# Kernel optimization log

Measured on AMD Instinct MI355X. Metric: run time of the kernel, lower is better.

The kernel has to match this reference:

```python
import jax, jax.numpy as jnp
import numpy as np

D_MODEL = 1024
N_HEADS = 16
D_FF = 4096
B = 8
S_TGT = 1024
S_SRC = 1024


def layer_norm(x, g, b, eps=1e-5):
    mu = jnp.mean(x, axis=-1, keepdims=True)
    var = jnp.mean(jnp.square(x - mu), axis=-1, keepdims=True)
    return (x - mu) * jax.lax.rsqrt(var + eps) * g + b


def mha(q_in, k_in, v_in, Wq, bq, Wk, bk, Wv, bv, Wo, bo, mask):
    Bq, Sq, D = q_in.shape
    hd = D // N_HEADS

    def split(t):
        return t.reshape(t.shape[0], t.shape[1], N_HEADS, hd).transpose(0, 2, 1, 3)

    Q = split(q_in @ Wq + bq)   # [B,H,Sq,hd]
    K = split(k_in @ Wk + bk)   # [B,H,Sk,hd]
    V = split(v_in @ Wv + bv)
    scores = jnp.einsum('bhqd,bhkd->bhqk', Q, K) / jnp.sqrt(jnp.float32(hd))
    scores = jnp.where(mask, scores, jnp.float32(-1e9))
    attn = jax.nn.softmax(scores, axis=-1)
    out = jnp.einsum('bhqk,bhkd->bhqd', attn, V)
    out = out.transpose(0, 2, 1, 3).reshape(Bq, Sq, D)
    return out @ Wo + bo


def setup_inputs() -> dict:
    key = jax.random.key(0)
    ks = jax.random.split(key, 32)
    s = 0.02
    inp = {
        'x': jax.random.normal(ks[0], (B, S_TGT, D_MODEL), dtype=jnp.float32),
        'encoder_output': jax.random.normal(ks[1], (B, S_SRC, D_MODEL), dtype=jnp.float32),
        'tgt_mask': jnp.tril(jnp.ones((S_TGT, S_TGT), dtype=bool))[None, None],
        'src_mask': jnp.ones((1, 1, S_TGT, S_SRC), dtype=bool),
    }
    i = 2
    for p in ('sa', 'ca'):
        for w in ('Wq', 'Wk', 'Wv', 'Wo'):
            inp[f'{p}_{w}'] = jax.random.normal(ks[i], (D_MODEL, D_MODEL), dtype=jnp.float32) * s
            inp[f'{p}_b{w[1].lower()}'] = jnp.zeros((D_MODEL,), dtype=jnp.float32)
            i += 1
    inp['ff_W1'] = jax.random.normal(ks[i], (D_MODEL, D_FF), dtype=jnp.float32) * s; i += 1
    inp['ff_b1'] = jnp.zeros((D_FF,), dtype=jnp.float32)
    inp['ff_W2'] = jax.random.normal(ks[i], (D_FF, D_MODEL), dtype=jnp.float32) * s; i += 1
    inp['ff_b2'] = jnp.zeros((D_MODEL,), dtype=jnp.float32)
    for n in ('ln1', 'ln2', 'ln3'):
        inp[f'{n}_g'] = jnp.ones((D_MODEL,), dtype=jnp.float32)
        inp[f'{n}_b'] = jnp.zeros((D_MODEL,), dtype=jnp.float32)
    return inp


def reference(x, encoder_output, tgt_mask, src_mask,
              sa_Wq, sa_bq, sa_Wk, sa_bk, sa_Wv, sa_bv, sa_Wo, sa_bo,
              ca_Wq, ca_bq, ca_Wk, ca_bk, ca_Wv, ca_bv, ca_Wo, ca_bo,
              ff_W1, ff_b1, ff_W2, ff_b2,
              ln1_g, ln1_b, ln2_g, ln2_b, ln3_g, ln3_b):
    # masked self-attention + residual + LN (dropout = identity in eval mode)
    attn = mha(x, x, x, sa_Wq, sa_bq, sa_Wk, sa_bk, sa_Wv, sa_bv, sa_Wo, sa_bo, tgt_mask)
    x = layer_norm(x + attn, ln1_g, ln1_b)
    # cross-attention to encoder output
    cross = mha(x, encoder_output, encoder_output,
                ca_Wq, ca_bq, ca_Wk, ca_bk, ca_Wv, ca_bv, ca_Wo, ca_bo, src_mask)
    x = layer_norm(x + cross, ln2_g, ln2_b)
    # position-wise FFN: Linear -> ReLU -> Linear
    ff = jax.nn.relu(x @ ff_W1 + ff_b1) @ ff_W2 + ff_b2
    x = layer_norm(x + ff, ln3_g, ln3_b)
    return x
```

## Files before the change

kernel.cpp:

```cpp
#include <hip/hip_runtime.h>
#include <math.h>

typedef __attribute__((ext_vector_type(8))) short short8;
typedef __attribute__((ext_vector_type(4))) short short4v;
typedef __attribute__((ext_vector_type(4))) float floatx4;

__device__ inline float bf2f(unsigned short h) {
    unsigned int u = ((unsigned int)h) << 16;
    float f;
    __builtin_memcpy(&f, &u, 4);
    return f;
}
__device__ inline unsigned short f2bf(float f) {
    unsigned int u;
    __builtin_memcpy(&u, &f, 4);
    u = (u + 0x7fffu + ((u >> 16) & 1u)) >> 16;
    return (unsigned short)u;
}
__device__ inline unsigned int f2u(float f) {
    return __builtin_bit_cast(unsigned int, f);
}

__device__ inline void gld_lds16(const unsigned short* g, unsigned short* l) {
    __builtin_amdgcn_global_load_lds(
        (const __attribute__((address_space(1))) unsigned int*)g,
        (__attribute__((address_space(3))) unsigned int*)l, 16, 0, 0);
}

__global__ __launch_bounds__(256) void detect_dtype(
    const unsigned short* __restrict__ x, int* __restrict__ flag) {
    __shared__ int s[4];
    int bad = 0;
    for (int i = threadIdx.x; i < 8192; i += 256) {
        float v = bf2f(x[i]);
        if (!(fabsf(v) <= 1.0e4f)) bad = 1;
    }
    unsigned long long b = __ballot(bad);
    int wave = threadIdx.x >> 6;
    if ((threadIdx.x & 63) == 0) s[wave] = (b != 0ULL) ? 1 : 0;
    __syncthreads();
    if (threadIdx.x == 0) flag[0] = s[0] | s[1] | s[2] | s[3];
}

__global__ __launch_bounds__(256) void to_bf16_kernel(
    const void* __restrict__ in, unsigned short* __restrict__ out,
    const int* __restrict__ flag, int n8) {
    int fl = flag[0];
    int i = blockIdx.x * 256 + threadIdx.x;
    if (i >= n8) return;
    size_t off = (size_t)i * 8;
    if (fl) {
        floatx4 f0 = *(const floatx4*)((const float*)in + off);
        floatx4 f1 = *(const floatx4*)((const float*)in + off + 4);
        short8 v;
#pragma unroll
        for (int j = 0; j < 4; j++) {
            v[j] = (short)f2bf(f0[j]);
            v[4 + j] = (short)f2bf(f1[j]);
        }
        *(short8*)(out + off) = v;
    } else {
        *(short8*)(out + off) = *(const short8*)((const unsigned short*)in + off);
    }
}

__global__ __launch_bounds__(256) void transpose_any(
    const void* __restrict__ in, unsigned short* __restrict__ out,
    int rows, int cols, const int* __restrict__ flag) {
    int fl = flag ? flag[0] : 0;
    __shared__ unsigned short t[32][33];
    int tx = threadIdx.x & 31, ty = threadIdx.x >> 5;
    int c0 = blockIdx.x * 32, r0 = blockIdx.y * 32;
    size_t base = (size_t)blockIdx.z * rows * cols;
#pragma unroll
    for (int k = 0; k < 4; k++) {
        size_t idx = base + (size_t)(r0 + ty + k * 8) * cols + c0 + tx;
        t[ty + k * 8][tx] = fl ? f2bf(((const float*)in)[idx])
                               : ((const unsigned short*)in)[idx];
    }
    __syncthreads();
#pragma unroll
    for (int k = 0; k < 4; k++)
        out[base + (size_t)(c0 + ty + k * 8) * rows + r0 + tx] = t[tx][ty + k * 8];
}

struct Ptr8 { const void* p[8]; };
__global__ __launch_bounds__(256) void transpose8(
    Ptr8 in, unsigned short* __restrict__ out, const int* __restrict__ flag) {
    int fl = flag[0];
    __shared__ unsigned short t[32][33];
    const void* src = in.p[blockIdx.z];
    unsigned short* dst = out + (size_t)blockIdx.z * 1024 * 1024;
    int tx = threadIdx.x & 31, ty = threadIdx.x >> 5;
    int c0 = blockIdx.x * 32, r0 = blockIdx.y * 32;
#pragma unroll
    for (int k = 0; k < 4; k++) {
        size_t idx = (size_t)(r0 + ty + k * 8) * 1024 + c0 + tx;
        t[ty + k * 8][tx] = fl ? f2bf(((const float*)src)[idx])
                               : ((const unsigned short*)src)[idx];
    }
    __syncthreads();
#pragma unroll
    for (int k = 0; k < 4; k++)
        dst[(size_t)(c0 + ty + k * 8) * 1024 + r0 + tx] = t[tx][ty + k * 8];
}

__device__ inline void stage_half(const unsigned short* __restrict__ G, int ldk,
                                  int grow, int gcol, unsigned short* ldsb,
                                  int tid) {
    int s0 = tid, s1 = tid + 512;
    int r0 = s0 >> 3, c0 = ((s0 & 7) ^ (r0 & 7)) << 3;
    int r1 = s1 >> 3, c1 = ((s1 & 7) ^ (r1 & 7)) << 3;
    gld_lds16(&G[(size_t)(grow + r0) * ldk + gcol + c0], &ldsb[s0 * 8]);
    gld_lds16(&G[(size_t)(grow + r1) * ldk + gcol + c1], &ldsb[s1 * 8]);
}

template <int BN_, int EPI>
__global__ __launch_bounds__(512) void gemm8(
    const unsigned short* __restrict__ A, const unsigned short* __restrict__ Bt,
    const void* __restrict__ b0, const void* __restrict__ b1,
    const void* __restrict__ b2, unsigned short* __restrict__ C0,
    unsigned short* __restrict__ C1, unsigned short* __restrict__ C2,
    int M, int N, int K, const int* __restrict__ flag) {
    constexpr int NR = BN_ / 64;
    constexpr int WNT = BN_ / 4;
    constexpr int ASZ = 16384;
    constexpr int BSZ = BN_ * 64;
    __shared__ alignas(16) unsigned short lds[2 * ASZ + 2 * BSZ];

    const int tid = threadIdx.x;
    const int lane = tid & 63, wave = tid >> 6;
    const int quad = lane >> 4, l16 = lane & 15, x7 = l16 & 7;
    const int wm = wave >> 2, wn = wave & 3;
    const int bm = blockIdx.x * 256, bn = blockIdx.y * BN_;
    const int NT = K >> 6;

    floatx4 acc[8][NR];
#pragma unroll
    for (int i = 0; i < 8; ++i)
#pragma unroll
        for (int j = 0; j < NR; ++j) acc[i][j] = (floatx4){0.f, 0.f, 0.f, 0.f};

    stage_half(A, K, bm, 0, lds, tid);
    stage_half(A, K, bm + 128, 0, lds + 8192, tid);
    stage_half(Bt, K, bn, 0, lds + 2 * ASZ, tid);
    if (BN_ == 256) stage_half(Bt, K, bn + 128, 0, lds + 2 * ASZ + 8192, tid);
    asm volatile("s_waitcnt vmcnt(0)" ::: "memory");
    __builtin_amdgcn_s_barrier();

    short8 bfr[NR][2], afr[2][2][2];

    for (int it = 0; it < NT; ++it) {
        unsigned short* const Ac = lds + (it & 1) * ASZ;
        unsigned short* const Bc = lds + 2 * ASZ + (it & 1) * BSZ;
        unsigned short* const An = lds + ((it + 1) & 1) * ASZ;
        unsigned short* const Bn = lds + 2 * ASZ + ((it + 1) & 1) * BSZ;
        const bool more = (it + 1 < NT);
        if (more) {
            const int kn = (it + 1) << 6;
            stage_half(A, K, bm, kn, An, tid);
            stage_half(A, K, bm + 128, kn, An + 8192, tid);
            stage_half(Bt, K, bn, kn, Bn, tid);
            if (BN_ == 256) stage_half(Bt, K, bn + 128, kn, Bn + 8192, tid);
        }
#pragma unroll
        for (int ni = 0; ni < NR; ++ni)
#pragma unroll
            for (int ks = 0; ks < 2; ++ks)
                bfr[ni][ks] = *(const short8*)&Bc[
                    (wn * WNT + ni * 16 + l16) * 64 +
                    ((((ks << 2) + quad) ^ x7) << 3)];
#pragma unroll
        for (int m2 = 0; m2 < 2; ++m2)
#pragma unroll
            for (int ks = 0; ks < 2; ++ks)
                afr[0][m2][ks] = *(const short8*)&Ac[
                    (wm * 128 + m2 * 16 + l16) * 64 +
                    ((((ks << 2) + quad) ^ x7) << 3)];
#pragma unroll
        for (int q = 0; q < 4; ++q) {
            if (q < 3) {
#pragma unroll
                for (int m2 = 0; m2 < 2; ++m2)
#pragma unroll
                    for (int ks = 0; ks < 2; ++ks)
                        afr[(q + 1) & 1][m2][ks] = *(const short8*)&Ac[
                            (wm * 128 + ((q + 1) * 2 + m2) * 16 + l16) * 64 +
                            ((((ks << 2) + quad) ^ x7) << 3)];
            }
            __builtin_amdgcn_s_setprio(1);
#pragma unroll
            for (int m2 = 0; m2 < 2; ++m2)
#pragma unroll
                for (int ni = 0; ni < NR; ++ni) {
                    acc[q * 2 + m2][ni] = __builtin_amdgcn_mfma_f32_16x16x32_bf16(
                        bfr[ni][0], afr[q & 1][m2][0], acc[q * 2 + m2][ni], 0, 0, 0);
                    acc[q * 2 + m2][ni] = __builtin_amdgcn_mfma_f32_16x16x32_bf16(
                        bfr[ni][1], afr[q & 1][m2][1], acc[q * 2 + m2][ni], 0, 0, 0);
                }
            __builtin_amdgcn_s_setprio(0);
        }
        if (more) {
            asm volatile("s_waitcnt vmcnt(0)" ::: "memory");
            __builtin_amdgcn_s_barrier();
        }
    }

    const int fl = flag[0];
    const void* bp = b0;
    unsigned short* Cp = C0;
    int mode = 0;
    int cb = bn;
    if (EPI == 1) mode = 1;
    if (EPI == 4) mode = 2;
    if (EPI == 2) {
        int ch = bn >> 10;
        cb = bn & 1023;
        bp = (ch == 0) ? b0 : (ch == 1) ? b1 : b2;
        Cp = (ch == 0) ? C0 : (ch == 1) ? C1 : C2;
        mode = (ch == 0) ? 2 : (ch == 1) ? 3 : 4;
    }
    if (EPI == 3) {
        int ch = bn >> 10;
        cb = bn & 1023;
        bp = (ch == 0) ? b0 : b1;
        Cp = (ch == 0) ? C0 : C1;
        mode = (ch == 0) ? 3 : 4;
    }
#pragma unroll
    for (int ni = 0; ni < NR; ++ni) {
        const int colb = cb + wn * WNT + ni * 16 + quad * 4;
        float b4[4];
        if (fl) {
            floatx4 t = *(const floatx4*)&((const float*)bp)[colb];
#pragma unroll
            for (int r = 0; r < 4; ++r) b4[r] = t[r];
        } else {
            short4v t = *(const short4v*)&((const unsigned short*)bp)[colb];
#pragma unroll
            for (int r = 0; r < 4; ++r) b4[r] = bf2f((unsigned short)t[r]);
        }
        const int hh = colb >> 6, dd = colb & 63;
#pragma unroll
        for (int mi = 0; mi < 8; ++mi) {
            const int row = bm + wm * 128 + mi * 16 + l16;
            short4v pk;
#pragma unroll
            for (int r = 0; r < 4; ++r) {
                float v = acc[mi][ni][r] + b4[r];
                if (mode == 1) v = fmaxf(v, 0.f);
                if (mode == 2) v *= 0.18033688f;
                pk[r] = (short)f2bf(v);
            }
            if (mode <= 1) {
                *(short4v*)&Cp[(size_t)row * N + colb] = pk;
            } else {
                const int b_ = row >> 10, s_ = row & 1023;
                if (mode != 4) {
                    *(short4v*)&Cp[((((size_t)b_ * 16 + hh) * 1024) + s_) * 64 + dd] = pk;
                } else {
#pragma unroll
                    for (int r = 0; r < 4; ++r)
                        Cp[(((size_t)b_ * 16 + hh) * 64 + dd + r) * 1024 + s_] =
                            (unsigned short)pk[r];
                }
            }
        }
    }
}

template <int CAUSAL>
__global__ __launch_bounds__(256) void attn_kernel(
    const unsigned short* __restrict__ Q, const unsigned short* __restrict__ K,
    const unsigned short* __restrict__ Vt, unsigned short* __restrict__ O,
    int Skv) {
    __shared__ alignas(16) unsigned short Ks[2][512 * 8];
    __shared__ alignas(16) unsigned short Vs[2][512 * 8];
    const int S = 1024;
    int tid = threadIdx.x, wave = tid >> 6, lane = tid & 63;
    int quad = lane >> 4, l16 = lane & 15;
    int fid = blockIdx.y * 8 + blockIdx.x;
    int bh = fid & 127;
    int qt = fid >> 7;
    if (CAUSAL) qt = 7 - qt;
    int qbA = qt * 128 + wave * 32;
    int qbB = qbA + 16;
    const unsigned short* Qp = Q + (size_t)bh * S * 64;
    const unsigned short* Kp = K + (size_t)bh * Skv * 64;
    const unsigned short* Vp = Vt + (size_t)bh * 64 * Skv;

    short8 qA0 = *(const short8*)&Qp[(qbA + l16) * 64 + quad * 8];
    short8 qA1 = *(const short8*)&Qp[(qbA + l16) * 64 + 32 + quad * 8];
    short8 qB0 = *(const short8*)&Qp[(qbB + l16) * 64 + quad * 8];
    short8 qB1 = *(const short8*)&Qp[(qbB + l16) * 64 + 32 + quad * 8];

    floatx4 oA[4], oB[4];
#pragma unroll
    for (int ni = 0; ni < 4; ni++) {
        oA[ni] = (floatx4){0.f, 0.f, 0.f, 0.f};
        oB[ni] = (floatx4){0.f, 0.f, 0.f, 0.f};
    }
    float mA = -1e30f, lA = 0.f, mB = -1e30f, lB = 0.f;
    const int kend = CAUSAL ? (qt + 1) * 128 : Skv;
    const int nch = kend >> 6;

    int sr0 = tid >> 3, sc0 = (tid & 7) ^ (sr0 & 7);
    int sr1 = (tid + 256) >> 3, sc1 = ((tid + 256) & 7) ^ (sr1 & 7);
    int shA = l16 + (((2 * quad) & 3) << 4);
    int shB = l16 + (((2 * quad + 1) & 3) << 4);

    short8 vone;
    {
        unsigned int dw[4] = {0x3F803F80u, 0x3F803F80u, 0x3F803F80u, 0x3F803F80u};
        __builtin_memcpy(&vone, dw, 16);
    }

    auto stageKV = [&](int kb, int b) {
        gld_lds16(&Kp[(size_t)(kb + sr0) * 64 + sc0 * 8], &Ks[b][tid * 8]);
        gld_lds16(&Kp[(size_t)(kb + sr1) * 64 + sc1 * 8], &Ks[b][(tid + 256) * 8]);
        gld_lds16(&Vp[(size_t)sr0 * Skv + kb + sc0 * 8], &Vs[b][tid * 8]);
        gld_lds16(&Vp[(size_t)sr1 * Skv + kb + sc1 * 8], &Vs[b][(tid + 256) * 8]);
    };

    stageKV(0, 0);
    asm volatile("s_waitcnt vmcnt(0)" ::: "memory");
    __builtin_amdgcn_s_barrier();

    for (int ic = 0; ic < nch; ++ic) {
        const int kb = ic << 6, cur = ic & 1;
        const unsigned short* Ksc = Ks[cur];
        const unsigned short* Vsc = Vs[cur];
        if (ic + 1 < nch) stageKV(kb + 64, cur ^ 1);

        const bool doA = !CAUSAL || (kb <= qbA + 15);
        const bool doB = !CAUSAL || (kb <= qbB + 15);

        if (doB) {
            floatx4 stA[4], stB[4];
            __builtin_amdgcn_s_setprio(1);
#pragma unroll
            for (int c = 0; c < 4; c++) {
                int row = c * 16 + l16, r7 = row & 7;
                short8 kf0 = *(const short8*)&Ksc[(row * 8 + (quad ^ r7)) * 8];
                short8 kf1 = *(const short8*)&Ksc[(row * 8 + ((quad + 4) ^ r7)) * 8];
                if (doA) {
                    floatx4 z = (floatx4){0.f, 0.f, 0.f, 0.f};
                    z = __builtin_amdgcn_mfma_f32_16x16x32_bf16(kf0, qA0, z, 0, 0, 0);
                    z = __builtin_amdgcn_mfma_f32_16x16x32_bf16(kf1, qA1, z, 0, 0, 0);
                    stA[c] = z;
                }
                floatx4 y = (floatx4){0.f, 0.f, 0.f, 0.f};
                y = __builtin_amdgcn_mfma_f32_16x16x32_bf16(kf0, qB0, y, 0, 0, 0);
                y = __builtin_amdgcn_mfma_f32_16x16x32_bf16(kf1, qB1, y, 0, 0, 0);
                stB[c] = y;
            }
            __builtin_amdgcn_s_setprio(0);

            auto softmax_pack = [&](floatx4(&st)[4], float& m, float& l,
                                    floatx4(&o)[4], short8(&pf)[2], int qb) {
                if (CAUSAL && (kb + 63 > qb)) {
#pragma unroll
                    for (int c = 0; c < 4; c++)
#pragma unroll
                        for (int r = 0; r < 4; r++) {
                            int kk = kb + c * 16 + quad * 4 + r;
                            if (kk > qb + l16) st[c][r] = -1e30f;
                        }
                }
                float t0 = fmaxf(fmaxf(st[0][0], st[0][1]), st[0][2]);
                float t1 = fmaxf(fmaxf(st[0][3], st[1][0]), st[1][1]);
                float t2 = fmaxf(fmaxf(st[1][2], st[1][3]), st[2][0]);
                float t3 = fmaxf(fmaxf(st[2][1], st[2][2]), st[2][3]);
                float t4 = fmaxf(fmaxf(st[3][0], st[3][1]), st[3][2]);
                float smax = fmaxf(fmaxf(fmaxf(t0, t1), fmaxf(t2, t3)),
                                   fmaxf(t4, st[3][3]));
                smax = fmaxf(smax, __shfl_xor(smax, 16));
                smax = fmaxf(smax, __shfl_xor(smax, 32));
                float mi = m;
                if (!__all(smax <= m + 8.f)) {
                    mi = fmaxf(m, smax);
                    float alpha = exp2f(m - mi);
                    l *= alpha;
#pragma unroll
                    for (int ni = 0; ni < 4; ni++) o[ni] *= alpha;
                    m = mi;
                }
#pragma unroll
                for (int c = 0; c < 4; c++)
#pragma unroll
                    for (int r = 0; r < 4; r++) st[c][r] = exp2f(st[c][r] - mi);
                unsigned int pd[4][2];
#pragma unroll
                for (int c = 0; c < 4; c++) {
                    pd[c][0] = __builtin_amdgcn_perm(f2u(st[c][1]), f2u(st[c][0]),
                                                     0x07060302u);
                    pd[c][1] = __builtin_amdgcn_perm(f2u(st[c][3]), f2u(st[c][2]),
                                                     0x07060302u);
                }
#pragma unroll
                for (int h = 0; h < 2; h++) {
                    unsigned int a0 = __shfl((int)pd[2 * h][0], shA);
                    unsigned int a1 = __shfl((int)pd[2 * h][1], shA);
                    unsigned int a2 = __shfl((int)pd[2 * h][0], shB);
                    unsigned int a3 = __shfl((int)pd[2 * h][1], shB);
                    unsigned int b0 = __shfl((int)pd[2 * h + 1][0], shA);
                    unsigned int b1 = __shfl((int)pd[2 * h + 1][1], shA);
                    unsigned int b2 = __shfl((int)pd[2 * h + 1][0], shB);
                    unsigned int b3 = __shfl((int)pd[2 * h + 1][1], shB);
                    unsigned int dw[4];
                    dw[0] = (quad < 2) ? a0 : b0;
                    dw[1] = (quad < 2) ? a1 : b1;
                    dw[2] = (quad < 2) ? a2 : b2;
                    dw[3] = (quad < 2) ? a3 : b3;
                    __builtin_memcpy(&pf[h], dw, 16);
                }
            };

            short8 pfA[2], pfB[2];
            if (doA) softmax_pack(stA, mA, lA, oA, pfA, qbA);
            softmax_pack(stB, mB, lB, oB, pfB, qbB);

            __builtin_amdgcn_s_setprio(1);
            if (doA) {
                floatx4 zA = (floatx4){0.f, 0.f, 0.f, 0.f};
                zA = __builtin_amdgcn_mfma_f32_16x16x32_bf16(vone, pfA[0], zA, 0, 0, 0);
                zA = __builtin_amdgcn_mfma_f32_16x16x32_bf16(vone, pfA[1], zA, 0, 0, 0);
                lA += zA[0];
            }
            {
                floatx4 zB = (floatx4){0.f, 0.f, 0.f, 0.f};
                zB = __builtin_amdgcn_mfma_f32_16x16x32_bf16(vone, pfB[0], zB, 0, 0, 0);
                zB = __builtin_amdgcn_mfma_f32_16x16x32_bf16(vone, pfB[1], zB, 0, 0, 0);
                lB += zB[0];
            }
#pragma unroll
            for (int ni = 0; ni < 4; ni++) {
                int row = ni * 16 + l16, r7 = row & 7;
                short8 vf0 = *(const short8*)&Vsc[(row * 8 + (quad ^ r7)) * 8];
                short8 vf1 = *(const short8*)&Vsc[(row * 8 + ((quad + 4) ^ r7)) * 8];
                if (doA) {
                    oA[ni] = __builtin_amdgcn_mfma_f32_16x16x32_bf16(vf0, pfA[0], oA[ni], 0, 0, 0);
                    oA[ni] = __builtin_amdgcn_mfma_f32_16x16x32_bf16(vf1, pfA[1], oA[ni], 0, 0, 0);
                }
                oB[ni] = __builtin_amdgcn_mfma_f32_16x16x32_bf16(vf0, pfB[0], oB[ni], 0, 0, 0);
                oB[ni] = __builtin_amdgcn_mfma_f32_16x16x32_bf16(vf1, pfB[1], oB[ni], 0, 0, 0);
            }
            __builtin_amdgcn_s_setprio(0);
        }

        if (ic + 1 < nch) {
            asm volatile("s_waitcnt vmcnt(0)" ::: "memory");
            __builtin_amdgcn_s_barrier();
        }
    }

    int b = bh >> 4, h = bh & 15;
    float invA = 1.0f / lA, invB = 1.0f / lB;
    size_t qrowA = ((size_t)(b * S + qbA + l16)) * 1024 + h * 64;
    size_t qrowB = ((size_t)(b * S + qbB + l16)) * 1024 + h * 64;
#pragma unroll
    for (int ni = 0; ni < 4; ni++) {
        short4v p4;
#pragma unroll
        for (int r = 0; r < 4; r++) p4[r] = (short)f2bf(oA[ni][r] * invA);
        *(short4v*)&O[qrowA + ni * 16 + quad * 4] = p4;
#pragma unroll
        for (int r = 0; r < 4; r++) p4[r] = (short)f2bf(oB[ni][r] * invB);
        *(short4v*)&O[qrowB + ni * 16 + quad * 4] = p4;
    }
}

template <int AEXT, int OEXT>
__global__ __launch_bounds__(256) void add_ln_kernel(
    const void* __restrict__ A, const unsigned short* __restrict__ Bv,
    const void* __restrict__ g, const void* __restrict__ be,
    void* __restrict__ out, const int* __restrict__ flag) {
    int fl = flag[0];
    __shared__ float red[2][4];
    int row = blockIdx.x, tid = threadIdx.x;
    size_t base = (size_t)row * 1024;
    int c = tid * 4;
    float v[4], sum = 0.f, ss = 0.f;
    if (AEXT && fl) {
        floatx4 af = *(const floatx4*)&((const float*)A)[base + c];
#pragma unroll
        for (int k = 0; k < 4; k++) v[k] = af[k];
    } else {
        short4v av = *(const short4v*)&((const unsigned short*)A)[base + c];
#pragma unroll
        for (int k = 0; k < 4; k++) v[k] = bf2f((unsigned short)av[k]);
    }
    short4v bv = *(const short4v*)&Bv[base + c];
#pragma unroll
    for (int k = 0; k < 4; k++) {
        v[k] += bf2f((unsigned short)bv[k]);
        sum += v[k];
        ss += v[k] * v[k];
    }
#pragma unroll
    for (int off = 1; off < 64; off <<= 1) {
        sum += __shfl_xor(sum, off);
        ss += __shfl_xor(ss, off);
    }
    int wave = tid >> 6, lane = tid & 63;
    if (lane == 0) {
        red[0][wave] = sum;
        red[1][wave] = ss;
    }
    __syncthreads();
    sum = red[0][0] + red[0][1] + red[0][2] + red[0][3];
    ss = red[1][0] + red[1][1] + red[1][2] + red[1][3];
    float mu = sum * (1.0f / 1024.0f);
    float var = ss * (1.0f / 1024.0f) - mu * mu;
    float rstd = rsqrtf(var + 1e-5f);
#pragma unroll
    for (int k = 0; k < 4; k++) {
        float gv = fl ? ((const float*)g)[c + k]
                      : bf2f(((const unsigned short*)g)[c + k]);
        float bev = fl ? ((const float*)be)[c + k]
                       : bf2f(((const unsigned short*)be)[c + k]);
        float y = (v[k] - mu) * rstd * gv + bev;
        if (OEXT && fl)
            ((float*)out)[base + c + k] = y;
        else
            ((unsigned short*)out)[base + c + k] = f2bf(y);
    }
}

extern "C" void kernel_launch(void* const* d_in, const int* in_sizes, int n_in,
                              void* d_out, int out_size, void* d_ws, size_t ws_size,
                              hipStream_t stream) {
    const int M = 8192;
    typedef const void* cvp;
    cvp x = d_in[0];
    cvp enc = d_in[1];
    cvp saWq = d_in[4], sabq = d_in[5];
    cvp saWk = d_in[6], sabk = d_in[7];
    cvp saWv = d_in[8], sabv = d_in[9];
    cvp saWo = d_in[10], sabo = d_in[11];
    cvp caWq = d_in[12], cabq = d_in[13];
    cvp caWk = d_in[14], cabk = d_in[15];
    cvp caWv = d_in[16], cabv = d_in[17];
    cvp caWo = d_in[18], cabo = d_in[19];
    cvp ffW1 = d_in[20], ffb1 = d_in[21];
    cvp ffW2 = d_in[22], ffb2 = d_in[23];
    cvp ln1g = d_in[24], ln1b = d_in[25];
    cvp ln2g = d_in[26], ln2b = d_in[27];
    cvp ln3g = d_in[28], ln3b = d_in[29];

    char* ws = (char*)d_ws;
    const size_t MB = 1024 * 1024;
    typedef unsigned short* up;
    up wt_sa_qkv = (up)(ws + 0);
    up wt_sa_o   = (up)(ws + 6 * MB);
    up wt_ca_q   = (up)(ws + 8 * MB);
    up wt_ca_kv  = (up)(ws + 10 * MB);
    up wt_ca_o   = (up)(ws + 14 * MB);
    up wtff1     = (up)(ws + 16 * MB);
    up wtff2     = (up)(ws + 24 * MB);
    up Qb  = (up)(ws + 32 * MB);
    up Kb  = (up)(ws + 48 * MB);
    up Vtb = (up)(ws + 64 * MB);
    up xb  = (up)(ws + 80 * MB);
    up Hb  = (up)(ws + 32 * MB);
    up Ob  = (up)(ws + 96 * MB);
    up Pb  = (up)(ws + 112 * MB);
    up x1  = (up)(ws + 128 * MB);
    up x2  = (up)(ws + 144 * MB);
    up encb = (up)(ws + 144 * MB);
    int* flag = (int*)(ws + 160 * MB);

    dim3 blk(256), blk5(512);
    detect_dtype<<<1, blk, 0, stream>>>((const unsigned short*)x, flag);

    to_bf16_kernel<<<4096, blk, 0, stream>>>(x, xb, flag, M * 1024 / 8);
    to_bf16_kernel<<<4096, blk, 0, stream>>>(enc, encb, flag, M * 1024 / 8);

    Ptr8 w8;
    w8.p[0] = saWq; w8.p[1] = saWk; w8.p[2] = saWv; w8.p[3] = saWo;
    w8.p[4] = caWq; w8.p[5] = caWk; w8.p[6] = caWv; w8.p[7] = caWo;
    transpose8<<<dim3(32, 32, 8), blk, 0, stream>>>(w8, (up)(ws + 0), flag);
    transpose_any<<<dim3(128, 32, 1), blk, 0, stream>>>(ffW1, wtff1, 1024, 4096, flag);
    transpose_any<<<dim3(32, 128, 1), blk, 0, stream>>>(ffW2, wtff2, 4096, 1024, flag);

    gemm8<256, 2><<<dim3(32, 12), blk5, 0, stream>>>(
        xb, wt_sa_qkv, sabq, sabk, sabv, Qb, Kb, Vtb, M, 3072, 1024, flag);
    attn_kernel<1><<<dim3(8, 128), blk, 0, stream>>>(Qb, Kb, Vtb, Ob, 1024);
    gemm8<128, 0><<<dim3(32, 8), blk5, 0, stream>>>(
        Ob, wt_sa_o, sabo, nullptr, nullptr, Pb, nullptr, nullptr, M, 1024, 1024, flag);
    add_ln_kernel<1, 0><<<dim3(8192), blk, 0, stream>>>(x, Pb, ln1g, ln1b, x1, flag);

    gemm8<128, 4><<<dim3(32, 8), blk5, 0, stream>>>(
        x1, wt_ca_q, cabq, nullptr, nullptr, Qb, nullptr, nullptr, M, 1024, 1024, flag);
    gemm8<256, 3><<<dim3(32, 8), blk5, 0, stream>>>(
        encb, wt_ca_kv, cabk, cabv, nullptr, Kb, Vtb, nullptr, M, 2048, 1024, flag);
    attn_kernel<0><<<dim3(8, 128), blk, 0, stream>>>(Qb, Kb, Vtb, Ob, 1024);
    gemm8<128, 0><<<dim3(32, 8), blk5, 0, stream>>>(
        Ob, wt_ca_o, cabo, nullptr, nullptr, Pb, nullptr, nullptr, M, 1024, 1024, flag);
    add_ln_kernel<0, 0><<<dim3(8192), blk, 0, stream>>>(x1, Pb, ln2g, ln2b, x2, flag);

    gemm8<256, 1><<<dim3(32, 16), blk5, 0, stream>>>(
        x2, wtff1, ffb1, nullptr, nullptr, Hb, nullptr, nullptr, M, 4096, 1024, flag);
    gemm8<128, 0><<<dim3(32, 8), blk5, 0, stream>>>(
        Hb, wtff2, ffb2, nullptr, nullptr, Pb, nullptr, nullptr, M, 1024, 4096, flag);
    add_ln_kernel<0, 1><<<dim3(8192), blk, 0, stream>>>(x2, Pb, ln3g, ln3b, d_out, flag);
}
```

Baseline: 783.9 us.

## Switch attention kernel to 32x32x16 MFMA tiles with a single 32-row query block per wave

Rewrites the flash-attention inner loop so each wave handles one 32-query tile using 32x32x16 bf16 MFMAs instead of two 16-row tiles with 16x16x32 MFMAs. The row sum l is now computed by in-register reductions rather than an extra MFMA against a ones vector. P fragments are repacked with a single xor-32 shuffle instead of indexed shuffles. The aim is fewer MFMA issues and fewer LDS fragment reads per tile. The costs are coarser causal skipping (32-row granularity) and higher accumulator register pressure.

```diff
diff --git a/kernel.cpp b/kernel.cpp
--- a/kernel.cpp
+++ b/kernel.cpp
@@ -4,6 +4,7 @@
 typedef __attribute__((ext_vector_type(8))) short short8;
 typedef __attribute__((ext_vector_type(4))) short short4v;
 typedef __attribute__((ext_vector_type(4))) float floatx4;
+typedef __attribute__((ext_vector_type(16))) float floatx16;
 
 __device__ inline float bf2f(unsigned short h) {
     unsigned int u = ((unsigned int)h) << 16;
@@ -278,42 +279,32 @@
     __shared__ alignas(16) unsigned short Vs[2][512 * 8];
     const int S = 1024;
     int tid = threadIdx.x, wave = tid >> 6, lane = tid & 63;
-    int quad = lane >> 4, l16 = lane & 15;
+    int h = lane >> 5, l31 = lane & 31;
     int fid = blockIdx.y * 8 + blockIdx.x;
     int bh = fid & 127;
     int qt = fid >> 7;
     if (CAUSAL) qt = 7 - qt;
-    int qbA = qt * 128 + wave * 32;
-    int qbB = qbA + 16;
+    const int qb = qt * 128 + wave * 32;
     const unsigned short* Qp = Q + (size_t)bh * S * 64;
     const unsigned short* Kp = K + (size_t)bh * Skv * 64;
     const unsigned short* Vp = Vt + (size_t)bh * 64 * Skv;
 
-    short8 qA0 = *(const short8*)&Qp[(qbA + l16) * 64 + quad * 8];
-    short8 qA1 = *(const short8*)&Qp[(qbA + l16) * 64 + 32 + quad * 8];
-    short8 qB0 = *(const short8*)&Qp[(qbB + l16) * 64 + quad * 8];
-    short8 qB1 = *(const short8*)&Qp[(qbB + l16) * 64 + 32 + quad * 8];
-
-    floatx4 oA[4], oB[4];
-#pragma unroll
-    for (int ni = 0; ni < 4; ni++) {
-        oA[ni] = (floatx4){0.f, 0.f, 0.f, 0.f};
-        oB[ni] = (floatx4){0.f, 0.f, 0.f, 0.f};
-    }
-    float mA = -1e30f, lA = 0.f, mB = -1e30f, lB = 0.f;
+    short8 qf[4];
+#pragma unroll
+    for (int t = 0; t < 4; t++)
+        qf[t] = *(const short8*)&Qp[(qb + l31) * 64 + t * 16 + h * 8];
+
+    floatx16 o[2];
+#pragma unroll
+    for (int dn = 0; dn < 2; dn++)
+#pragma unroll
+        for (int rr = 0; rr < 16; rr++) o[dn][rr] = 0.f;
+    float m = -1e30f, l = 0.f;
     const int kend = CAUSAL ? (qt + 1) * 128 : Skv;
     const int nch = kend >> 6;
 
     int sr0 = tid >> 3, sc0 = (tid & 7) ^ (sr0 & 7);
     int sr1 = (tid + 256) >> 3, sc1 = ((tid + 256) & 7) ^ (sr1 & 7);
-    int shA = l16 + (((2 * quad) & 3) << 4);
-    int shB = l16 + (((2 * quad + 1) & 3) << 4);
-
-    short8 vone;
-    {
-        unsigned int dw[4] = {0x3F803F80u, 0x3F803F80u, 0x3F803F80u, 0x3F803F80u};
-        __builtin_memcpy(&vone, dw, 16);
-    }
 
     auto stageKV = [&](int kb, int b) {
         gld_lds16(&Kp[(size_t)(kb + sr0) * 64 + sc0 * 8], &Ks[b][tid * 8]);
@@ -332,119 +323,107 @@
         const unsigned short* Vsc = Vs[cur];
         if (ic + 1 < nch) stageKV(kb + 64, cur ^ 1);
 
-        const bool doA = !CAUSAL || (kb <= qbA + 15);
-        const bool doB = !CAUSAL || (kb <= qbB + 15);
-
-        if (doB) {
-            floatx4 stA[4], stB[4];
+        const bool act = !CAUSAL || (kb <= qb + 31);
+        if (act) {
+            floatx16 st[2];
             __builtin_amdgcn_s_setprio(1);
 #pragma unroll
-            for (int c = 0; c < 4; c++) {
-                int row = c * 16 + l16, r7 = row & 7;
-                short8 kf0 = *(const short8*)&Ksc[(row * 8 + (quad ^ r7)) * 8];
-                short8 kf1 = *(const short8*)&Ksc[(row * 8 + ((quad + 4) ^ r7)) * 8];
-                if (doA) {
-                    floatx4 z = (floatx4){0.f, 0.f, 0.f, 0.f};
-                    z = __builtin_amdgcn_mfma_f32_16x16x32_bf16(kf0, qA0, z, 0, 0, 0);
-                    z = __builtin_amdgcn_mfma_f32_16x16x32_bf16(kf1, qA1, z, 0, 0, 0);
-                    stA[c] = z;
+            for (int kg = 0; kg < 2; kg++) {
+                const int row = kg * 32 + l31, r7 = row & 7;
+                floatx16 z;
+#pragma unroll
+                for (int rr = 0; rr < 16; rr++) z[rr] = 0.f;
+#pragma unroll
+                for (int t = 0; t < 4; t++) {
+                    short8 kf = *(const short8*)&Ksc[
+                        (row * 8 + ((2 * t + h) ^ r7)) * 8];
+                    z = __builtin_amdgcn_mfma_f32_32x32x16_bf16(kf, qf[t], z,
+                                                                0, 0, 0);
                 }
-                floatx4 y = (floatx4){0.f, 0.f, 0.f, 0.f};
-                y = __builtin_amdgcn_mfma_f32_16x16x32_bf16(kf0, qB0, y, 0, 0, 0);
-                y = __builtin_amdgcn_mfma_f32_16x16x32_bf16(kf1, qB1, y, 0, 0, 0);
-                stB[c] = y;
+                st[kg] = z;
             }
             __builtin_amdgcn_s_setprio(0);
 
-            auto softmax_pack = [&](floatx4(&st)[4], float& m, float& l,
-                                    floatx4(&o)[4], short8(&pf)[2], int qb) {
-                if (CAUSAL && (kb + 63 > qb)) {
-#pragma unroll
-                    for (int c = 0; c < 4; c++)
-#pragma unroll
-                        for (int r = 0; r < 4; r++) {
-                            int kk = kb + c * 16 + quad * 4 + r;
-                            if (kk > qb + l16) st[c][r] = -1e30f;
-                        }
+            if (CAUSAL && (kb + 63 > qb)) {
+#pragma unroll
+                for (int kg = 0; kg < 2; kg++)
+#pragma unroll
+                    for (int rr = 0; rr < 16; rr++) {
+                        int key = kb + kg * 32 + (rr & 3) + 8 * (rr >> 2) + 4 * h;
+                        if (key > qb + l31) st[kg][rr] = -1e30f;
+                    }
+            }
+            float mx[16];
+#pragma unroll
+            for (int rr = 0; rr < 16; rr++) mx[rr] = fmaxf(st[0][rr], st[1][rr]);
+#pragma unroll
+            for (int s2 = 8; s2 > 0; s2 >>= 1)
+#pragma unroll
+                for (int rr = 0; rr < s2; rr++)
+                    mx[rr] = fmaxf(mx[rr], mx[rr + s2]);
+            float smax = fmaxf(mx[0], __shfl_xor(mx[0], 32));
+            float mi = m;
+            if (!__all(smax <= m + 8.f)) {
+                mi = fmaxf(m, smax);
+                float alpha = exp2f(m - mi);
+                l *= alpha;
+#pragma unroll
+                for (int dn = 0; dn < 2; dn++)
+#pragma unroll
+                    for (int rr = 0; rr < 16; rr++) o[dn][rr] *= alpha;
+                m = mi;
+            }
+#pragma unroll
+            for (int kg = 0; kg < 2; kg++)
+#pragma unroll
+                for (int rr = 0; rr < 16; rr++)
+                    st[kg][rr] = exp2f(st[kg][rr] - mi);
+            float sm[16];
+#pragma unroll
+            for (int rr = 0; rr < 16; rr++) sm[rr] = st[0][rr] + st[1][rr];
+#pragma unroll
+            for (int s2 = 8; s2 > 0; s2 >>= 1)
+#pragma unroll
+                for (int rr = 0; rr < s2; rr++) sm[rr] += sm[rr + s2];
+            l += sm[0] + __shfl_xor(sm[0], 32);
+
+            unsigned int pd[2][4][2];
+#pragma unroll
+            for (int kg = 0; kg < 2; kg++)
+#pragma unroll
+                for (int g = 0; g < 4; g++)
+#pragma unroll
+                    for (int i = 0; i < 2; i++)
+                        pd[kg][g][i] = __builtin_amdgcn_perm(
+                            f2u(st[kg][4 * g + 2 * i + 1]),
+                            f2u(st[kg][4 * g + 2 * i]), 0x07060302u);
+
+            __builtin_amdgcn_s_setprio(1);
+#pragma unroll
+            for (int kg = 0; kg < 2; kg++)
+#pragma unroll
+                for (int kt = 0; kt < 2; kt++) {
+                    unsigned int dw[4];
+#pragma unroll
+                    for (int i = 0; i < 2; i++) {
+                        unsigned int a = pd[kg][2 * kt][i];
+                        unsigned int b_ = pd[kg][2 * kt + 1][i];
+                        unsigned int ax = (unsigned int)__shfl_xor((int)a, 32);
+                        unsigned int bx = (unsigned int)__shfl_xor((int)b_, 32);
+                        dw[i] = h ? bx : a;
+                        dw[2 + i] = h ? b_ : ax;
+                    }
+                    short8 pf;
+                    __builtin_memcpy(&pf, dw, 16);
+#pragma unroll
+                    for (int dn = 0; dn < 2; dn++) {
+                        const int row = dn * 32 + l31, r7 = row & 7;
+                        short8 vf = *(const short8*)&Vsc[
+                            (row * 8 + ((kg * 4 + 2 * kt + h) ^ r7)) * 8];
+                        o[dn] = __builtin_amdgcn_mfma_f32_32x32x16_bf16(
+                            vf, pf, o[dn], 0, 0, 0);
+                    }
                 }
-                float t0 = fmaxf(fmaxf(st[0][0], st[0][1]), st[0][2]);
-                float t1 = fmaxf(fmaxf(st[0][3], st[1][0]), st[1][1]);
-                float t2 = fmaxf(fmaxf(st[1][2], st[1][3]), st[2][0]);
-                float t3 = fmaxf(fmaxf(st[2][1], st[2][2]), st[2][3]);
-                float t4 = fmaxf(fmaxf(st[3][0], st[3][1]), st[3][2]);
-                float smax = fmaxf(fmaxf(fmaxf(t0, t1), fmaxf(t2, t3)),
-                                   fmaxf(t4, st[3][3]));
-                smax = fmaxf(smax, __shfl_xor(smax, 16));
-                smax = fmaxf(smax, __shfl_xor(smax, 32));
-                float mi = m;
-                if (!__all(smax <= m + 8.f)) {
-                    mi = fmaxf(m, smax);
-                    float alpha = exp2f(m - mi);
-                    l *= alpha;
-#pragma unroll
-                    for (int ni = 0; ni < 4; ni++) o[ni] *= alpha;
-                    m = mi;
-                }
-#pragma unroll
-                for (int c = 0; c < 4; c++)
-#pragma unroll
-                    for (int r = 0; r < 4; r++) st[c][r] = exp2f(st[c][r] - mi);
-                unsigned int pd[4][2];
-#pragma unroll
-                for (int c = 0; c < 4; c++) {
-                    pd[c][0] = __builtin_amdgcn_perm(f2u(st[c][1]), f2u(st[c][0]),
-                                                     0x07060302u);
-                    pd[c][1] = __builtin_amdgcn_perm(f2u(st[c][3]), f2u(st[c][2]),
-                                                     0x07060302u);
-                }
-#pragma unroll
-                for (int h = 0; h < 2; h++) {
-                    unsigned int a0 = __shfl((int)pd[2 * h][0], shA);
-                    unsigned int a1 = __shfl((int)pd[2 * h][1], shA);
-                    unsigned int a2 = __shfl((int)pd[2 * h][0], shB);
-                    unsigned int a3 = __shfl((int)pd[2 * h][1], shB);
-                    unsigned int b0 = __shfl((int)pd[2 * h + 1][0], shA);
-                    unsigned int b1 = __shfl((int)pd[2 * h + 1][1], shA);
-                    unsigned int b2 = __shfl((int)pd[2 * h + 1][0], shB);
-                    unsigned int b3 = __shfl((int)pd[2 * h + 1][1], shB);
-                    unsigned int dw[4];
-                    dw[0] = (quad < 2) ? a0 : b0;
-                    dw[1] = (quad < 2) ? a1 : b1;
-                    dw[2] = (quad < 2) ? a2 : b2;
-                    dw[3] = (quad < 2) ? a3 : b3;
-                    __builtin_memcpy(&pf[h], dw, 16);
-                }
-            };
-
-            short8 pfA[2], pfB[2];
-            if (doA) softmax_pack(stA, mA, lA, oA, pfA, qbA);
-            softmax_pack(stB, mB, lB, oB, pfB, qbB);
-
-            __builtin_amdgcn_s_setprio(1);
-            if (doA) {
-                floatx4 zA = (floatx4){0.f, 0.f, 0.f, 0.f};
-                zA = __builtin_amdgcn_mfma_f32_16x16x32_bf16(vone, pfA[0], zA, 0, 0, 0);
-                zA = __builtin_amdgcn_mfma_f32_16x16x32_bf16(vone, pfA[1], zA, 0, 0, 0);
-                lA += zA[0];
-            }
-            {
-                floatx4 zB = (floatx4){0.f, 0.f, 0.f, 0.f};
-                zB = __builtin_amdgcn_mfma_f32_16x16x32_bf16(vone, pfB[0], zB, 0, 0, 0);
-                zB = __builtin_amdgcn_mfma_f32_16x16x32_bf16(vone, pfB[1], zB, 0, 0, 0);
-                lB += zB[0];
-            }
-#pragma unroll
-            for (int ni = 0; ni < 4; ni++) {
-                int row = ni * 16 + l16, r7 = row & 7;
-                short8 vf0 = *(const short8*)&Vsc[(row * 8 + (quad ^ r7)) * 8];
-                short8 vf1 = *(const short8*)&Vsc[(row * 8 + ((quad + 4) ^ r7)) * 8];
-                if (doA) {
-                    oA[ni] = __builtin_amdgcn_mfma_f32_16x16x32_bf16(vf0, pfA[0], oA[ni], 0, 0, 0);
-                    oA[ni] = __builtin_amdgcn_mfma_f32_16x16x32_bf16(vf1, pfA[1], oA[ni], 0, 0, 0);
-                }
-                oB[ni] = __builtin_amdgcn_mfma_f32_16x16x32_bf16(vf0, pfB[0], oB[ni], 0, 0, 0);
-                oB[ni] = __builtin_amdgcn_mfma_f32_16x16x32_bf16(vf1, pfB[1], oB[ni], 0, 0, 0);
-            }
             __builtin_amdgcn_s_setprio(0);
         }
 
@@ -454,20 +433,19 @@
         }
     }
 
-    int b = bh >> 4, h = bh & 15;
-    float invA = 1.0f / lA, invB = 1.0f / lB;
-    size_t qrowA = ((size_t)(b * S + qbA + l16)) * 1024 + h * 64;
-    size_t qrowB = ((size_t)(b * S + qbB + l16)) * 1024 + h * 64;
-#pragma unroll
-    for (int ni = 0; ni < 4; ni++) {
-        short4v p4;
-#pragma unroll
-        for (int r = 0; r < 4; r++) p4[r] = (short)f2bf(oA[ni][r] * invA);
-        *(short4v*)&O[qrowA + ni * 16 + quad * 4] = p4;
-#pragma unroll
-        for (int r = 0; r < 4; r++) p4[r] = (short)f2bf(oB[ni][r] * invB);
-        *(short4v*)&O[qrowB + ni * 16 + quad * 4] = p4;
-    }
+    int b = bh >> 4, hh = bh & 15;
+    float inv = 1.0f / l;
+    size_t orow = ((size_t)(b * S + qb + l31)) * 1024 + hh * 64;
+#pragma unroll
+    for (int dn = 0; dn < 2; dn++)
+#pragma unroll
+        for (int g = 0; g < 4; g++) {
+            short4v p4;
+#pragma unroll
+            for (int r = 0; r < 4; r++)
+                p4[r] = (short)f2bf(o[dn][4 * g + r] * inv);
+            *(short4v*)&O[orow + dn * 32 + 8 * g + 4 * h] = p4;
+        }
 }
 
 template <int AEXT, int OEXT>
```

Measured after the change: 775.4 us. About the same (-1.1%).
